# Performance work log

Hardware: AMD Instinct MI355X
Metric: run time of the kernel (lower is better)

Reference implementation:

```python
import jax, jax.numpy as jnp
import numpy as np

N_NODES = 100000
N_EDGES = 3200000
N_GRAPHS = 4096
N_REL = 5
N_BASES = 4
HID = 32


def setup_inputs() -> dict:
    key = jax.random.key(0)
    ks = jax.random.split(key, 32)
    inp = {}
    inp['x'] = jax.random.normal(ks[0], (N_NODES, 4), dtype=jnp.float32)
    inp['edge_index'] = jax.random.randint(ks[1], (2, N_EDGES), 0, N_NODES, dtype=jnp.int64)
    inp['edge_type'] = jax.random.randint(ks[2], (N_EDGES,), 0, N_REL, dtype=jnp.int64)
    inp['user_idx'] = jax.random.randint(ks[3], (N_GRAPHS,), 0, N_NODES, dtype=jnp.int64)
    inp['item_idx'] = jax.random.randint(ks[4], (N_GRAPHS,), 0, N_NODES, dtype=jnp.int64)
    k = 5
    for l in range(4):
        in_c = 4 if l == 0 else HID
        inp[f'basis{l}'] = jax.random.normal(ks[k], (N_BASES, in_c, HID), dtype=jnp.float32) * 0.1; k += 1
        inp[f'comp{l}'] = jax.random.normal(ks[k], (N_REL, N_BASES), dtype=jnp.float32) * 0.5; k += 1
        inp[f'root{l}'] = jax.random.normal(ks[k], (in_c, HID), dtype=jnp.float32) * 0.1; k += 1
        inp[f'bias{l}'] = jax.random.normal(ks[k], (HID,), dtype=jnp.float32) * 0.01; k += 1
    inp['w1'] = jax.random.normal(ks[k], (256, 128), dtype=jnp.float32) * 0.05; k += 1
    inp['b1'] = jnp.zeros((128,), dtype=jnp.float32)
    inp['w2'] = jax.random.normal(ks[k], (128, 1), dtype=jnp.float32) * 0.05; k += 1
    inp['b2'] = jnp.zeros((1,), dtype=jnp.float32)
    return inp


def _rgcn_layer(x, src, key5, inv_cnt, basis, comp, root, bias, n_nodes):
    # mean-aggregate raw source features per (dst, relation): [N, R, in]
    agg = jax.ops.segment_sum(x[src], key5, num_segments=n_nodes * N_REL)
    agg = agg.reshape(n_nodes, N_REL, -1) * inv_cnt
    # basis-decomposed relation weights: W_r = sum_b comp[r,b] * basis[b]
    w = jnp.einsum('rb,bio->rio', comp, basis)  # [R, in, out]
    return jnp.einsum('nri,rio->no', agg, w) + x @ root + bias


def reference(x, edge_index, edge_type, user_idx, item_idx,
              basis0, comp0, root0, bias0,
              basis1, comp1, root1, bias1,
              basis2, comp2, root2, bias2,
              basis3, comp3, root3, bias3,
              w1, b1, w2, b2):
    n_nodes = x.shape[0]
    src, dst = edge_index[0], edge_index[1]
    key5 = dst * N_REL + edge_type  # combined (dst, relation) segment id
    cnt = jax.ops.segment_sum(jnp.ones_like(edge_type, dtype=x.dtype), key5,
                              num_segments=n_nodes * N_REL)
    inv_cnt = (1.0 / jnp.maximum(cnt, 1.0)).reshape(n_nodes, N_REL, 1)
    params = [(basis0, comp0, root0, bias0), (basis1, comp1, root1, bias1),
              (basis2, comp2, root2, bias2), (basis3, comp3, root3, bias3)]
    out = x
    hs = []
    for (basis, comp, root, bias) in params:
        out = jnp.tanh(_rgcn_layer(out, src, key5, inv_cnt, basis, comp, root, bias, n_nodes))
        hs.append(out)
    h = jnp.concatenate(hs, axis=1)            # [N, 128]
    g = jnp.concatenate([h[user_idx], h[item_idx]], axis=1)  # [B, 256]
    z = jax.nn.relu(g @ w1 + b1)
    return (z @ w2 + b2)[:, 0]
```

## Files before the change

### kernel.cpp

```cpp
#include <hip/hip_runtime.h>
#include <hip/hip_bf16.h>
#include <hip/hip_fp16.h>

#define N_NODES 100000
#define N_EDGES 3200000
#define N_GRAPHS 4096
#define N_REL 5
#define N_BASES 4
#define HID 32
#define SEG (N_NODES*N_REL)
#define DUMMY N_NODES

#define NBUCK 392
#define BCAP  10240
#define PBCAP 15360
#define NKEY  1280
#define PTILE 4096

#define KDIM 192
#define ASTR 208

typedef _Float16 half8 __attribute__((ext_vector_type(8)));
typedef float floatx4 __attribute__((ext_vector_type(4)));

static __global__ __launch_bounds__(256) void k_part(const int* __restrict__ ei,
                                                     const int* __restrict__ et,
                                                     int* __restrict__ gcur,
                                                     unsigned long long* __restrict__ part) {
    __shared__ unsigned long long stage[PTILE];
    __shared__ int hist[NBUCK];
    __shared__ int lofs[NBUCK];
    __shared__ int lbase[NBUCK];
    __shared__ int sscan[256];
    int t = threadIdx.x;
    int e0 = blockIdx.x * PTILE;
    int tile_n = N_EDGES - e0; if (tile_n > PTILE) tile_n = PTILE;

    for (int k = t; k < NBUCK; k += 256) hist[k] = 0;
    __syncthreads();
    int src[16], bkt[16], lkey[16];
#pragma unroll
    for (int j = 0; j < 16; j++) {
        int e = e0 + j * 256 + t;
        if (e < N_EDGES) {
            int s = ei[e];
            int d = ei[N_EDGES + e];
            int r = et[e];
            src[j] = s; bkt[j] = d >> 8; lkey[j] = ((d & 255) * 5) + r;
            atomicAdd(&hist[bkt[j]], 1);
        } else bkt[j] = -1;
    }
    __syncthreads();
    int h0 = (2 * t     < NBUCK) ? hist[2 * t]     : 0;
    int h1 = (2 * t + 1 < NBUCK) ? hist[2 * t + 1] : 0;
    int s2 = h0 + h1;
    sscan[t] = s2;
    __syncthreads();
    for (int off = 1; off < 256; off <<= 1) {
        int xv = (t >= off) ? sscan[t - off] : 0;
        __syncthreads();
        sscan[t] += xv;
        __syncthreads();
    }
    int excl = sscan[t] - s2;
    if (2 * t     < NBUCK) lofs[2 * t]     = excl;
    if (2 * t + 1 < NBUCK) lofs[2 * t + 1] = excl + h0;
    for (int k = t; k < NBUCK; k += 256) lbase[k] = atomicAdd(&gcur[k], hist[k]);
    __syncthreads();
    for (int k = t; k < NBUCK; k += 256) hist[k] = 0;
    __syncthreads();
#pragma unroll
    for (int j = 0; j < 16; j++) {
        if (bkt[j] >= 0) {
            int rank = atomicAdd(&hist[bkt[j]], 1);
            stage[lofs[bkt[j]] + rank] =
                ((unsigned long long)(unsigned)((bkt[j] << 16) | lkey[j]) << 32)
                | (unsigned)src[j];
        }
    }
    __syncthreads();
    for (int i = t; i < tile_n; i += 256) {
        unsigned long long u = stage[i];
        unsigned hi = (unsigned)(u >> 32);
        int bb = hi >> 16;
        unsigned long long lk = hi & 0xFFFFu;
        int pos = lbase[bb] + (i - lofs[bb]);
        if (pos < BCAP)
            part[(size_t)bb * BCAP + pos] = (lk << 32) | (u & 0xffffffffULL);
    }
}

static __global__ __launch_bounds__(1024) void k_bsort(const unsigned long long* __restrict__ part,
                                                       const int* __restrict__ gcur,
                                                       int* __restrict__ offs,
                                                       int* __restrict__ cnt,
                                                       int* __restrict__ srcs) {
    __shared__ int lhist[NKEY];
    __shared__ int lscan[NKEY];
    __shared__ int sscan[256];
    __shared__ int lsrc[PBCAP];
    int b = blockIdx.x;
    int t = threadIdx.x;
    int n = gcur[b]; if (n > BCAP) n = BCAP;
    const unsigned long long* reg = part + (size_t)b * BCAP;

    for (int k = t; k < NKEY; k += 1024) lhist[k] = 0;
    __syncthreads();
    for (int i = t; i < n; i += 1024)
        atomicAdd(&lhist[(int)(reg[i] >> 32)], 1);
    __syncthreads();

    int loc[5]; int s5 = 0;
    if (t < 256) {
#pragma unroll
        for (int j = 0; j < 5; j++) { loc[j] = s5; s5 += (lhist[t * 5 + j] + 7) & ~7; }
        sscan[t] = s5;
    }
    __syncthreads();
    for (int off = 1; off < 256; off <<= 1) {
        int x = (t >= off && t < 256) ? sscan[t - off] : 0;
        __syncthreads();
        if (t < 256) sscan[t] += x;
        __syncthreads();
    }
    if (t < 256) {
        int excl = sscan[t] - s5;
#pragma unroll
        for (int j = 0; j < 5; j++) lscan[t * 5 + j] = excl + loc[j];
    }
    __syncthreads();
    int ptot = sscan[255]; if (ptot > PBCAP) ptot = PBCAP;
    int pout = ptot + 16; if (pout > PBCAP) pout = PBCAP;

    int base = b * PBCAP;
    if (t < 256) {
#pragma unroll
        for (int j = 0; j < 5; j++) {
            int k = t * 5 + j;
            int segid = b * NKEY + k;
            if (segid < SEG) {
                cnt[segid]  = lhist[k];
                offs[segid] = base + lscan[k];
            }
        }
    }
    __syncthreads();
    for (int k = t; k < NKEY; k += 1024) lhist[k] = 0;
    for (int i = t; i < pout; i += 1024) lsrc[i] = DUMMY;
    __syncthreads();
    for (int i = t; i < n; i += 1024) {
        unsigned long long u = reg[i];
        int k = (int)(u >> 32);
        int pos = lscan[k] + atomicAdd(&lhist[k], 1);
        if (pos < PBCAP) lsrc[pos] = (int)(u & 0xffffffffULL);
    }
    __syncthreads();
    for (int i = t; i < pout; i += 1024) srcs[base + i] = lsrc[i];
}

static __global__ __launch_bounds__(256) void k_pad(const float* __restrict__ x,
                                                    __half* __restrict__ ht0,
                                                    __half* __restrict__ ht1,
                                                    __half* __restrict__ ht2,
                                                    __half* __restrict__ ht3,
                                                    __half* __restrict__ ht4,
                                                    int* __restrict__ srcs) {
    int tid = blockIdx.x * 256 + threadIdx.x;
    if (tid < (N_NODES + 1) * 32) {
        int nd = tid >> 5, ii = tid & 31;
        float v = (nd < N_NODES && ii < 4) ? x[(nd << 2) + ii] : 0.f;
        ht0[tid] = __float2half(v);
    } else {
        int r = tid - (N_NODES + 1) * 32;
        if (r < 128) {
            __half* hp = (r < 32) ? ht1 : (r < 64) ? ht2 : (r < 96) ? ht3 : ht4;
            hp[N_NODES * 32 + (r & 31)] = __float2half(0.f);
        } else if (r < 144) srcs[NBUCK * PBCAP + (r - 128)] = DUMMY;
    }
}

static __global__ __launch_bounds__(256) void k_wprepB(
    const float* __restrict__ ba0, const float* __restrict__ co0, const float* __restrict__ ro0,
    const float* __restrict__ ba1, const float* __restrict__ co1, const float* __restrict__ ro1,
    const float* __restrict__ ba2, const float* __restrict__ co2, const float* __restrict__ ro2,
    const float* __restrict__ ba3, const float* __restrict__ co3, const float* __restrict__ ro3,
    __half* __restrict__ Wb) {
    int idx = blockIdx.x * 256 + threadIdx.x;
    int j    = idx & 7;
    int lane = (idx >> 3) & 63;
    int tile = (idx >> 9) & 1;
    int ls   = idx >> 10;
    int l    = ls / 6;
    int s    = ls - l * 6;
    const float* basis = (l == 0) ? ba0 : (l == 1) ? ba1 : (l == 2) ? ba2 : ba3;
    const float* comp  = (l == 0) ? co0 : (l == 1) ? co1 : (l == 2) ? co2 : co3;
    const float* root  = (l == 0) ? ro0 : (l == 1) ? ro1 : (l == 2) ? ro2 : ro3;
    int in_c = (l == 0) ? 4 : HID;
    int d = ((lane >> 4) << 3) + j;
    int o = tile * 16 + (lane & 15);
    float v = 0.f;
    if (d < in_c) {
        if (s < 5) {
            float acc = 0.f;
#pragma unroll
            for (int b = 0; b < N_BASES; b++)
                acc += comp[s * N_BASES + b] * basis[(b * in_c + d) * HID + o];
            v = acc;
        } else {
            v = root[d * HID + o];
        }
    }
    Wb[idx] = __float2half(v);
}

static __global__ __launch_bounds__(256) void k_wprepM(const float* __restrict__ w1,
                                                       __half* __restrict__ Wm) {
    int idx = blockIdx.x * 256 + threadIdx.x;
    int j    = idx & 7;
    int lane = (idx >> 3) & 63;
    int s    = (idx >> 9) & 7;
    int tile = idx >> 12;
    int k = s * 32 + ((lane >> 4) << 3) + j;
    int o = tile * 16 + (lane & 15);
    Wm[idx] = __float2half(w1[k * 128 + o]);
}

static __global__ __launch_bounds__(256, 6) void k_layer(
    const __half* __restrict__ tab, const int* __restrict__ offs,
    const int* __restrict__ cnt, const int* __restrict__ srcs,
    const __half* __restrict__ Wbl, const float* __restrict__ bias,
    __half* __restrict__ hout) {
    __shared__ __align__(16) __half sAgg[64 * ASTR];
    int t = threadIdx.x;
    int wave = t >> 6, lane = t & 63;
    int nsub = lane >> 2, cp = lane & 3;
    int nl = wave * 16 + nsub;
    int n = blockIdx.x * 64 + nl;
    int nn = (n < N_NODES) ? n : (N_NODES - 1);
    const half8* tab8 = (const half8*)tab;

    int s5 = nn * N_REL;
    int o0 = offs[s5];
    int cc[5];
#pragma unroll
    for (int r = 0; r < 5; r++) cc[r] = cnt[s5 + r];

    __half* row = sAgg + nl * ASTR;
    half8 selfv = tab8[nn * 4 + cp];
    *(half8*)(row + 160 + cp * 8) = selfv;

    int orun = o0;
#pragma unroll
    for (int r = 0; r < 5; r++) {
        int cr = cc[r];
        int pr = (cr + 7) & ~7;
        const int* sp = srcs + orun;
        int4 e0 = *(const int4*)(sp);
        int4 e1 = *(const int4*)(sp + 4);
        half8 g0 = tab8[e0.x * 4 + cp], g1 = tab8[e0.y * 4 + cp];
        half8 g2 = tab8[e0.z * 4 + cp], g3 = tab8[e0.w * 4 + cp];
        half8 g4 = tab8[e1.x * 4 + cp], g5 = tab8[e1.y * 4 + cp];
        half8 g6 = tab8[e1.z * 4 + cp], g7 = tab8[e1.w * 4 + cp];
        half8 sb = ((g0 + g1) + (g2 + g3)) + ((g4 + g5) + (g6 + g7));
        float S0 = (float)sb[0], S1 = (float)sb[1], S2 = (float)sb[2], S3 = (float)sb[3];
        float S4 = (float)sb[4], S5 = (float)sb[5], S6 = (float)sb[6], S7 = (float)sb[7];
        for (int s8 = 8; s8 < pr; s8 += 8) {
            int4 f0 = *(const int4*)(sp + s8);
            int4 f1 = *(const int4*)(sp + s8 + 4);
            half8 h0 = tab8[f0.x * 4 + cp], h1 = tab8[f0.y * 4 + cp];
            half8 h2 = tab8[f0.z * 4 + cp], h3 = tab8[f0.w * 4 + cp];
            half8 h4 = tab8[f1.x * 4 + cp], h5 = tab8[f1.y * 4 + cp];
            half8 h6 = tab8[f1.z * 4 + cp], h7 = tab8[f1.w * 4 + cp];
            half8 rb = ((h0 + h1) + (h2 + h3)) + ((h4 + h5) + (h6 + h7));
            S0 += (float)rb[0]; S1 += (float)rb[1]; S2 += (float)rb[2]; S3 += (float)rb[3];
            S4 += (float)rb[4]; S5 += (float)rb[5]; S6 += (float)rb[6]; S7 += (float)rb[7];
        }
        float ic = (cr > 0) ? __builtin_amdgcn_rcpf((float)cr) : 0.f;
        half8 u;
        u[0] = (_Float16)(S0 * ic); u[1] = (_Float16)(S1 * ic);
        u[2] = (_Float16)(S2 * ic); u[3] = (_Float16)(S3 * ic);
        u[4] = (_Float16)(S4 * ic); u[5] = (_Float16)(S5 * ic);
        u[6] = (_Float16)(S6 * ic); u[7] = (_Float16)(S7 * ic);
        *(half8*)(row + r * 32 + cp * 8) = u;
        orun += pr;
    }
    __syncthreads();

    floatx4 acc0 = {0.f, 0.f, 0.f, 0.f}, acc1 = {0.f, 0.f, 0.f, 0.f};
    const __half* aBase = sAgg + (wave * 16 + (lane & 15)) * ASTR + ((lane >> 4) << 3);
    const __half* bBase = Wbl + lane * 8;
#pragma unroll
    for (int s = 0; s < 6; s++) {
        half8 a  = *(const half8*)(aBase + s * 32);
        half8 f0 = *(const half8*)(bBase + (s * 2 + 0) * 512);
        half8 f1 = *(const half8*)(bBase + (s * 2 + 1) * 512);
        acc0 = __builtin_amdgcn_mfma_f32_16x16x32_f16(a, f0, acc0, 0, 0, 0);
        acc1 = __builtin_amdgcn_mfma_f32_16x16x32_f16(a, f1, acc1, 0, 0, 0);
    }
    int oc = lane & 15;
    float bi0 = bias[oc], bi1 = bias[16 + oc];
#pragma unroll
    for (int r = 0; r < 4; r++) {
        int node = blockIdx.x * 64 + wave * 16 + ((lane >> 4) << 2) + r;
        if (node < N_NODES) {
            hout[node * 32 + oc]      = __float2half(tanhf(acc0[r] + bi0));
            hout[node * 32 + 16 + oc] = __float2half(tanhf(acc1[r] + bi1));
        }
    }
}

static __global__ __launch_bounds__(256) void k_mlp(
    const __half* __restrict__ h1, const __half* __restrict__ h2,
    const __half* __restrict__ h3, const __half* __restrict__ h4,
    const int* __restrict__ uidx, const int* __restrict__ iidx,
    const __half* __restrict__ Wm, const float* __restrict__ b1,
    const float* __restrict__ w2, const float* __restrict__ b2,
    float* __restrict__ out) {
    __shared__ __align__(16) __half sg[16 * 264];
    __shared__ float sacc[4][16];
    int t = threadIdx.x, wave = t >> 6, lane = t & 63;
    int g0 = blockIdx.x * 16;
    int lt = lane >> 4, lp = lane & 15;
    const __half* htab = (lt == 0) ? h1 : (lt == 1) ? h2 : (lt == 2) ? h3 : h4;
#pragma unroll
    for (int gg2 = 0; gg2 < 4; gg2++) {
        int gg = wave * 4 + gg2;
        int g = g0 + gg;
        int u = uidx[g], it = iidx[g];
        __half2* dst = (__half2*)(sg + gg * 264);
        dst[lt * 16 + lp]      = ((const __half2*)(htab + u * 32))[lp];
        dst[64 + lt * 16 + lp] = ((const __half2*)(htab + it * 32))[lp];
    }
    __syncthreads();
    floatx4 acc0 = {0.f, 0.f, 0.f, 0.f}, acc1 = {0.f, 0.f, 0.f, 0.f};
    const __half* aBase = sg + (lane & 15) * 264 + ((lane >> 4) << 3);
    const __half* bB0 = Wm + (wave * 2 + 0) * 4096 + lane * 8;
    const __half* bB1 = Wm + (wave * 2 + 1) * 4096 + lane * 8;
#pragma unroll
    for (int s = 0; s < 8; s++) {
        half8 a  = *(const half8*)(aBase + s * 32);
        half8 f0 = *(const half8*)(bB0 + s * 512);
        half8 f1 = *(const half8*)(bB1 + s * 512);
        acc0 = __builtin_amdgcn_mfma_f32_16x16x32_f16(a, f0, acc0, 0, 0, 0);
        acc1 = __builtin_amdgcn_mfma_f32_16x16x32_f16(a, f1, acc1, 0, 0, 0);
    }
    int o0 = wave * 32 + (lane & 15);
    int o1 = o0 + 16;
    float b10 = b1[o0], b11 = b1[o1], w20 = w2[o0], w21 = w2[o1];
#pragma unroll
    for (int r = 0; r < 4; r++) {
        float z0 = fmaxf(acc0[r] + b10, 0.f);
        float z1 = fmaxf(acc1[r] + b11, 0.f);
        float v = z0 * w20 + z1 * w21;
#pragma unroll
        for (int off = 1; off < 16; off <<= 1) v += __shfl_xor(v, off);
        if ((lane & 15) == 0) sacc[wave][((lane >> 4) << 2) + r] = v;
    }
    __syncthreads();
    if (t < 16)
        out[g0 + t] = sacc[0][t] + sacc[1][t] + sacc[2][t] + sacc[3][t] + b2[0];
}

extern "C" void kernel_launch(void* const* d_in, const int* in_sizes, int n_in,
                              void* d_out, int out_size, void* d_ws, size_t ws_size,
                              hipStream_t stream) {
    const float* x  = (const float*)d_in[0];
    const int*   ei = (const int*)d_in[1];
    const int*   et = (const int*)d_in[2];
    const int*   ui = (const int*)d_in[3];
    const int*   ii = (const int*)d_in[4];
    const float* w1 = (const float*)d_in[21];
    const float* b1 = (const float*)d_in[22];
    const float* w2 = (const float*)d_in[23];
    const float* b2 = (const float*)d_in[24];

    char* ws = (char*)d_ws;
    if (ws_size < 92167680UL) return;
    int*    gcur = (int*)(ws + 0);
    int*    offs = (int*)(ws + 2048);
    int*    cnt  = (int*)(ws + 2002176);
    int*    srcs = (int*)(ws + 4002304);
    __half* Wb   = (__half*)(ws + 28086912);
    __half* Wm   = (__half*)(ws + 28136064);
    __half* ht0  = (__half*)(ws + 28201600);
    __half* ht1  = (__half*)(ws + 34601728);
    __half* ht2  = (__half*)(ws + 41001856);
    __half* ht3  = (__half*)(ws + 47401984);
    __half* ht4  = (__half*)(ws + 53802112);
    unsigned long long* part = (unsigned long long*)(ws + 34601728);

    hipMemsetAsync(gcur, 0, NBUCK * 4, stream);

    k_part<<<(N_EDGES + PTILE - 1) / PTILE, 256, 0, stream>>>(ei, et, gcur, part);
    k_bsort<<<NBUCK, 1024, 0, stream>>>(part, gcur, offs, cnt, srcs);
    k_pad<<<12501, 256, 0, stream>>>(x, ht0, ht1, ht2, ht3, ht4, srcs);
    k_wprepB<<<96, 256, 0, stream>>>(
        (const float*)d_in[5],  (const float*)d_in[6],  (const float*)d_in[7],
        (const float*)d_in[9],  (const float*)d_in[10], (const float*)d_in[11],
        (const float*)d_in[13], (const float*)d_in[14], (const float*)d_in[15],
        (const float*)d_in[17], (const float*)d_in[18], (const float*)d_in[19], Wb);
    k_wprepM<<<128, 256, 0, stream>>>(w1, Wm);

    __half* tabs[5] = {ht0, ht1, ht2, ht3, ht4};
    for (int l = 0; l < 4; l++) {
        const float* bias = (const float*)d_in[8 + 4 * l];
        k_layer<<<(N_NODES + 63) / 64, 256, 0, stream>>>(
            tabs[l], offs, cnt, srcs, Wb + l * 6144, bias, tabs[l + 1]);
    }
    k_mlp<<<256, 256, 0, stream>>>(ht1, ht2, ht3, ht4, ui, ii, Wm, b1, w2, b2,
                                   (float*)d_out);
}
```

Baseline: 361.3 us.

## Merge prep kernels, shrink layer blocks to 32 nodes, prefetch edge indices

Combines the padding, basis-weight and MLP-weight preparation kernels into one launch to cut launch overhead. The layer kernel moves from 64-node, 256-thread blocks to 32-node, 128-thread blocks (launch bounds 128,5), giving more blocks and a smaller LDS footprint. It also loads the first eight source indices of all five relations up front so the gather loads can be issued together, and drops the bounds guards because N_NODES divides evenly by 32. The extra live registers from the prefetched indices may lower occupancy.

Result: faster. 335.5 us (-7.1%).

```diff
diff --git a/kernel.cpp b/kernel.cpp
--- a/kernel.cpp
+++ b/kernel.cpp
@@ -158,109 +158,113 @@
     for (int i = t; i < pout; i += 1024) srcs[base + i] = lsrc[i];
 }
 
-static __global__ __launch_bounds__(256) void k_pad(const float* __restrict__ x,
-                                                    __half* __restrict__ ht0,
-                                                    __half* __restrict__ ht1,
-                                                    __half* __restrict__ ht2,
-                                                    __half* __restrict__ ht3,
-                                                    __half* __restrict__ ht4,
-                                                    int* __restrict__ srcs) {
-    int tid = blockIdx.x * 256 + threadIdx.x;
-    if (tid < (N_NODES + 1) * 32) {
-        int nd = tid >> 5, ii = tid & 31;
-        float v = (nd < N_NODES && ii < 4) ? x[(nd << 2) + ii] : 0.f;
-        ht0[tid] = __float2half(v);
-    } else {
-        int r = tid - (N_NODES + 1) * 32;
-        if (r < 128) {
-            __half* hp = (r < 32) ? ht1 : (r < 64) ? ht2 : (r < 96) ? ht3 : ht4;
-            hp[N_NODES * 32 + (r & 31)] = __float2half(0.f);
-        } else if (r < 144) srcs[NBUCK * PBCAP + (r - 128)] = DUMMY;
-    }
-}
-
-static __global__ __launch_bounds__(256) void k_wprepB(
+static __global__ __launch_bounds__(256) void k_prep(
+    const float* __restrict__ x,
+    __half* __restrict__ ht0, __half* __restrict__ ht1, __half* __restrict__ ht2,
+    __half* __restrict__ ht3, __half* __restrict__ ht4, int* __restrict__ srcs,
     const float* __restrict__ ba0, const float* __restrict__ co0, const float* __restrict__ ro0,
     const float* __restrict__ ba1, const float* __restrict__ co1, const float* __restrict__ ro1,
     const float* __restrict__ ba2, const float* __restrict__ co2, const float* __restrict__ ro2,
     const float* __restrict__ ba3, const float* __restrict__ co3, const float* __restrict__ ro3,
-    __half* __restrict__ Wb) {
-    int idx = blockIdx.x * 256 + threadIdx.x;
-    int j    = idx & 7;
-    int lane = (idx >> 3) & 63;
-    int tile = (idx >> 9) & 1;
-    int ls   = idx >> 10;
-    int l    = ls / 6;
-    int s    = ls - l * 6;
-    const float* basis = (l == 0) ? ba0 : (l == 1) ? ba1 : (l == 2) ? ba2 : ba3;
-    const float* comp  = (l == 0) ? co0 : (l == 1) ? co1 : (l == 2) ? co2 : co3;
-    const float* root  = (l == 0) ? ro0 : (l == 1) ? ro1 : (l == 2) ? ro2 : ro3;
-    int in_c = (l == 0) ? 4 : HID;
-    int d = ((lane >> 4) << 3) + j;
-    int o = tile * 16 + (lane & 15);
-    float v = 0.f;
-    if (d < in_c) {
-        if (s < 5) {
-            float acc = 0.f;
-#pragma unroll
-            for (int b = 0; b < N_BASES; b++)
-                acc += comp[s * N_BASES + b] * basis[(b * in_c + d) * HID + o];
-            v = acc;
+    __half* __restrict__ Wb, const float* __restrict__ w1, __half* __restrict__ Wm) {
+    int blk = blockIdx.x;
+    int t = threadIdx.x;
+    if (blk < 12501) {
+        int tid = blk * 256 + t;
+        if (tid < (N_NODES + 1) * 32) {
+            int nd = tid >> 5, ii = tid & 31;
+            float v = (nd < N_NODES && ii < 4) ? x[(nd << 2) + ii] : 0.f;
+            ht0[tid] = __float2half(v);
         } else {
-            v = root[d * HID + o];
+            int r = tid - (N_NODES + 1) * 32;
+            if (r < 128) {
+                __half* hp = (r < 32) ? ht1 : (r < 64) ? ht2 : (r < 96) ? ht3 : ht4;
+                hp[N_NODES * 32 + (r & 31)] = __float2half(0.f);
+            } else if (r < 144) srcs[NBUCK * PBCAP + (r - 128)] = DUMMY;
         }
-    }
-    Wb[idx] = __float2half(v);
-}
-
-static __global__ __launch_bounds__(256) void k_wprepM(const float* __restrict__ w1,
-                                                       __half* __restrict__ Wm) {
-    int idx = blockIdx.x * 256 + threadIdx.x;
-    int j    = idx & 7;
-    int lane = (idx >> 3) & 63;
-    int s    = (idx >> 9) & 7;
-    int tile = idx >> 12;
-    int k = s * 32 + ((lane >> 4) << 3) + j;
-    int o = tile * 16 + (lane & 15);
-    Wm[idx] = __float2half(w1[k * 128 + o]);
-}
-
-static __global__ __launch_bounds__(256, 6) void k_layer(
+    } else if (blk < 12501 + 96) {
+        int idx = (blk - 12501) * 256 + t;
+        int j    = idx & 7;
+        int lane = (idx >> 3) & 63;
+        int tile = (idx >> 9) & 1;
+        int ls   = idx >> 10;
+        int l    = ls / 6;
+        int s    = ls - l * 6;
+        const float* basis = (l == 0) ? ba0 : (l == 1) ? ba1 : (l == 2) ? ba2 : ba3;
+        const float* comp  = (l == 0) ? co0 : (l == 1) ? co1 : (l == 2) ? co2 : co3;
+        const float* root  = (l == 0) ? ro0 : (l == 1) ? ro1 : (l == 2) ? ro2 : ro3;
+        int in_c = (l == 0) ? 4 : HID;
+        int d = ((lane >> 4) << 3) + j;
+        int o = tile * 16 + (lane & 15);
+        float v = 0.f;
+        if (d < in_c) {
+            if (s < 5) {
+                float acc = 0.f;
+#pragma unroll
+                for (int b = 0; b < N_BASES; b++)
+                    acc += comp[s * N_BASES + b] * basis[(b * in_c + d) * HID + o];
+                v = acc;
+            } else {
+                v = root[d * HID + o];
+            }
+        }
+        Wb[idx] = __float2half(v);
+    } else {
+        int idx = (blk - 12597) * 256 + t;
+        int j    = idx & 7;
+        int lane = (idx >> 3) & 63;
+        int s    = (idx >> 9) & 7;
+        int tile = idx >> 12;
+        int k = s * 32 + ((lane >> 4) << 3) + j;
+        int o = tile * 16 + (lane & 15);
+        Wm[idx] = __float2half(w1[k * 128 + o]);
+    }
+}
+
+static __global__ __launch_bounds__(128, 5) void k_layer(
     const __half* __restrict__ tab, const int* __restrict__ offs,
     const int* __restrict__ cnt, const int* __restrict__ srcs,
     const __half* __restrict__ Wbl, const float* __restrict__ bias,
     __half* __restrict__ hout) {
-    __shared__ __align__(16) __half sAgg[64 * ASTR];
+    __shared__ __align__(16) __half sAgg[32 * ASTR];
     int t = threadIdx.x;
     int wave = t >> 6, lane = t & 63;
     int nsub = lane >> 2, cp = lane & 3;
     int nl = wave * 16 + nsub;
-    int n = blockIdx.x * 64 + nl;
-    int nn = (n < N_NODES) ? n : (N_NODES - 1);
+    int n = blockIdx.x * 32 + nl;
     const half8* tab8 = (const half8*)tab;
 
-    int s5 = nn * N_REL;
+    int s5 = n * N_REL;
     int o0 = offs[s5];
     int cc[5];
 #pragma unroll
     for (int r = 0; r < 5; r++) cc[r] = cnt[s5 + r];
 
     __half* row = sAgg + nl * ASTR;
-    half8 selfv = tab8[nn * 4 + cp];
-    *(half8*)(row + 160 + cp * 8) = selfv;
-
-    int orun = o0;
+    *(half8*)(row + 160 + cp * 8) = tab8[n * 4 + cp];
+
+    int ob[5];
+    {
+        int orun = o0;
+#pragma unroll
+        for (int r = 0; r < 5; r++) { ob[r] = orun; orun += (cc[r] + 7) & ~7; }
+    }
+    int4 E0[5], E1[5];
+#pragma unroll
+    for (int r = 0; r < 5; r++) {
+        const int* sp = srcs + ob[r];
+        E0[r] = *(const int4*)(sp);
+        E1[r] = *(const int4*)(sp + 4);
+    }
 #pragma unroll
     for (int r = 0; r < 5; r++) {
         int cr = cc[r];
         int pr = (cr + 7) & ~7;
-        const int* sp = srcs + orun;
-        int4 e0 = *(const int4*)(sp);
-        int4 e1 = *(const int4*)(sp + 4);
-        half8 g0 = tab8[e0.x * 4 + cp], g1 = tab8[e0.y * 4 + cp];
-        half8 g2 = tab8[e0.z * 4 + cp], g3 = tab8[e0.w * 4 + cp];
-        half8 g4 = tab8[e1.x * 4 + cp], g5 = tab8[e1.y * 4 + cp];
-        half8 g6 = tab8[e1.z * 4 + cp], g7 = tab8[e1.w * 4 + cp];
+        const int* sp = srcs + ob[r];
+        half8 g0 = tab8[E0[r].x * 4 + cp], g1 = tab8[E0[r].y * 4 + cp];
+        half8 g2 = tab8[E0[r].z * 4 + cp], g3 = tab8[E0[r].w * 4 + cp];
+        half8 g4 = tab8[E1[r].x * 4 + cp], g5 = tab8[E1[r].y * 4 + cp];
+        half8 g6 = tab8[E1[r].z * 4 + cp], g7 = tab8[E1[r].w * 4 + cp];
         half8 sb = ((g0 + g1) + (g2 + g3)) + ((g4 + g5) + (g6 + g7));
         float S0 = (float)sb[0], S1 = (float)sb[1], S2 = (float)sb[2], S3 = (float)sb[3];
         float S4 = (float)sb[4], S5 = (float)sb[5], S6 = (float)sb[6], S7 = (float)sb[7];
@@ -282,7 +286,6 @@
         u[4] = (_Float16)(S4 * ic); u[5] = (_Float16)(S5 * ic);
         u[6] = (_Float16)(S6 * ic); u[7] = (_Float16)(S7 * ic);
         *(half8*)(row + r * 32 + cp * 8) = u;
-        orun += pr;
     }
     __syncthreads();
 
@@ -301,11 +304,9 @@
     float bi0 = bias[oc], bi1 = bias[16 + oc];
 #pragma unroll
     for (int r = 0; r < 4; r++) {
-        int node = blockIdx.x * 64 + wave * 16 + ((lane >> 4) << 2) + r;
-        if (node < N_NODES) {
-            hout[node * 32 + oc]      = __float2half(tanhf(acc0[r] + bi0));
-            hout[node * 32 + 16 + oc] = __float2half(tanhf(acc1[r] + bi1));
-        }
+        int node = blockIdx.x * 32 + wave * 16 + ((lane >> 4) << 2) + r;
+        hout[node * 32 + oc]      = __float2half(tanhf(acc0[r] + bi0));
+        hout[node * 32 + 16 + oc] = __float2half(tanhf(acc1[r] + bi1));
     }
 }
 
@@ -393,18 +394,18 @@
 
     k_part<<<(N_EDGES + PTILE - 1) / PTILE, 256, 0, stream>>>(ei, et, gcur, part);
     k_bsort<<<NBUCK, 1024, 0, stream>>>(part, gcur, offs, cnt, srcs);
-    k_pad<<<12501, 256, 0, stream>>>(x, ht0, ht1, ht2, ht3, ht4, srcs);
-    k_wprepB<<<96, 256, 0, stream>>>(
+    k_prep<<<12725, 256, 0, stream>>>(
+        x, ht0, ht1, ht2, ht3, ht4, srcs,
         (const float*)d_in[5],  (const float*)d_in[6],  (const float*)d_in[7],
         (const float*)d_in[9],  (const float*)d_in[10], (const float*)d_in[11],
         (const float*)d_in[13], (const float*)d_in[14], (const float*)d_in[15],
-        (const float*)d_in[17], (const float*)d_in[18], (const float*)d_in[19], Wb);
-    k_wprepM<<<128, 256, 0, stream>>>(w1, Wm);
+        (const float*)d_in[17], (const float*)d_in[18], (const float*)d_in[19],
+        Wb, w1, Wm);
 
     __half* tabs[5] = {ht0, ht1, ht2, ht3, ht4};
     for (int l = 0; l < 4; l++) {
         const float* bias = (const float*)d_in[8 + 4 * l];
-        k_layer<<<(N_NODES + 63) / 64, 256, 0, stream>>>(
+        k_layer<<<N_NODES / 32, 128, 0, stream>>>(
             tabs[l], offs, cnt, srcs, Wb + l * 6144, bias, tabs[l + 1]);
     }
     k_mlp<<<256, 256, 0, stream>>>(ht1, ht2, ht3, ht4, ui, ii, Wm, b1, w2, b2,
```
